# Performance work log

Measured on AMD Instinct MI355X. Metric: run time of the kernel, lower is better.

Reference implementation:

```python
import jax, jax.numpy as jnp
import numpy as np

NUM_HEADS = 16
NUM_KV_HEADS = 4
HEAD_DIM = 128
MAX_LEN = 1024
SEQ_LENS = [1024, 896, 768, 640, 1024, 512, 960, 704]
SCALE = HEAD_DIM ** -0.5
NEG_INF = -1e10  # matches the Triton kernel's masking constant


def setup_inputs() -> dict:
    key = jax.random.key(0)
    kq, kk, kv = jax.random.split(key, 3)
    total = int(np.sum(SEQ_LENS))  # 6528 ragged tokens
    q = jax.random.normal(kq, (total, NUM_HEADS, HEAD_DIM), dtype=jnp.float32)
    k = jax.random.normal(kk, (total, NUM_KV_HEADS, HEAD_DIM), dtype=jnp.float32)
    v = jax.random.normal(kv, (total, NUM_KV_HEADS, HEAD_DIM), dtype=jnp.float32)
    cu_seqlens = jnp.asarray(np.concatenate([[0], np.cumsum(SEQ_LENS)]), dtype=jnp.int32)
    return {"q": q, "k": k, "v": v, "cu_seqlens": cu_seqlens}


def _varlen_flash_attention(q, k, v, cu_seqlens):
    # q: [T, H, D]; k, v: [T, KVH, D]; cu_seqlens: [B+1]
    T, H, D = q.shape
    KVH = k.shape[1]
    g = H // KVH  # GQA group size; head h reads kv head h // g (consecutive groups)
    lens = cu_seqlens[1:] - cu_seqlens[:-1]                 # [B]
    pos = jnp.arange(MAX_LEN)
    idx = cu_seqlens[:-1, None] + pos[None, :]              # [B, L] ragged -> padded gather indices
    valid = pos[None, :] < lens[:, None]                    # [B, L]
    idx = jnp.where(valid, idx, 0)
    qp = q[idx]                                             # [B, L, H, D]
    kp = jnp.repeat(k[idx], g, axis=2)                      # [B, L, H, D]
    vp = jnp.repeat(v[idx], g, axis=2)                      # [B, L, H, D]
    scores = jnp.einsum('blhd,bmhd->bhlm', qp, kp) * SCALE  # [B, H, L, L]
    causal = pos[:, None] >= pos[None, :]                   # [L, L]
    mask = causal[None, None, :, :] & valid[:, None, None, :]
    scores = jnp.where(mask, scores, NEG_INF)
    p = jax.nn.softmax(scores, axis=-1)                     # stable online-softmax equivalent
    op = jnp.einsum('bhlm,bmhd->blhd', p, vp)               # [B, L, H, D]
    op = op * valid[..., None, None]                        # zero padded query rows
    # scatter padded output back to ragged layout (each valid idx is unique)
    out = jnp.zeros_like(q).at[idx.reshape(-1)].add(op.reshape(-1, H, D))
    return out


def reference(q, k, v, cu_seqlens):
    return _varlen_flash_attention(q, k, v, cu_seqlens)
```

## Files before the change

### kernel.cpp

```cpp
#include <hip/hip_runtime.h>
#include <stdint.h>


#define NH 16
#define NKVH 4
#define HD 128
#define NB 8
#define SCALE 0.08838834764831844f
#define NEG_INF -1.0e10f
#define NT32 204
#define TILE_IMG 32768
#define WS_NEED ((size_t)NKVH * NT32 * TILE_IMG)

typedef short bf16x8 __attribute__((ext_vector_type(8)));
typedef float f32x16 __attribute__((ext_vector_type(16)));
typedef unsigned short us4 __attribute__((ext_vector_type(4)));
typedef unsigned short us8 __attribute__((ext_vector_type(8)));

union FragU { us8 u; bf16x8 b; };

__device__ __forceinline__ unsigned short f2bf(float f) {
    uint32_t u = __float_as_uint(f);
    u += 0x7fffu + ((u >> 16) & 1u);
    return (unsigned short)(u >> 16);
}
__device__ __forceinline__ float bf2f(unsigned short h) {
    return __uint_as_float(((uint32_t)h) << 16);
}

__constant__ int c_s32[NB] = {0, 32, 60, 84, 104, 136, 152, 182};
__constant__ signed char c_b[NT32] = {
  0,4, 0,4, 0,4,6, 0,4,6, 0,1,4,6, 0,1,4,6, 0,1,4,6, 0,1,4,6,
  0,1,2,4,6, 0,1,2,4,6, 0,1,2,4,6,7, 0,1,2,4,6,7,
  0,1,2,3,4,6,7, 0,1,2,3,4,6,7, 0,1,2,3,4,6,7, 0,1,2,3,4,6,7,
  0,1,2,3,4,5,6,7, 0,1,2,3,4,5,6,7, 0,1,2,3,4,5,6,7, 0,1,2,3,4,5,6,7,
  0,1,2,3,4,5,6,7, 0,1,2,3,4,5,6,7, 0,1,2,3,4,5,6,7, 0,1,2,3,4,5,6,7,
  0,1,2,3,4,5,6,7, 0,1,2,3,4,5,6,7, 0,1,2,3,4,5,6,7, 0,1,2,3,4,5,6,7,
  0,1,2,3,4,5,6,7, 0,1,2,3,4,5,6,7, 0,1,2,3,4,5,6,7, 0,1,2,3,4,5,6,7};
__constant__ signed char c_qt[NT32] = {
  31,31, 30,30, 29,29,29, 28,28,28, 27,27,27,27, 26,26,26,26, 25,25,25,25,
  24,24,24,24, 23,23,23,23,23, 22,22,22,22,22, 21,21,21,21,21,21,
  20,20,20,20,20,20, 19,19,19,19,19,19,19, 18,18,18,18,18,18,18,
  17,17,17,17,17,17,17, 16,16,16,16,16,16,16,
  15,15,15,15,15,15,15,15, 14,14,14,14,14,14,14,14, 13,13,13,13,13,13,13,13,
  12,12,12,12,12,12,12,12, 11,11,11,11,11,11,11,11, 10,10,10,10,10,10,10,10,
  9,9,9,9,9,9,9,9, 8,8,8,8,8,8,8,8, 7,7,7,7,7,7,7,7, 6,6,6,6,6,6,6,6,
  5,5,5,5,5,5,5,5, 4,4,4,4,4,4,4,4, 3,3,3,3,3,3,3,3, 2,2,2,2,2,2,2,2,
  1,1,1,1,1,1,1,1, 0,0,0,0,0,0,0,0};

__global__ __launch_bounds__(256, 4)
void prepack(const float* __restrict__ K, const float* __restrict__ V,
             unsigned char* __restrict__ ws)
{
    const int gt  = blockIdx.x;
    const int kvh = blockIdx.y;
    const int tid = threadIdx.x;
    unsigned char* img = ws + ((size_t)(kvh * NT32 + gt)) * TILE_IMG;

    #pragma unroll
    for (int i = 0; i < 4; ++i) {
        int chunk = tid + 256 * i;
        int key = chunk >> 5, dq = chunk & 31;
        const float* kp = K + ((size_t)(gt * 32 + key) * NKVH + kvh) * HD + dq * 4;
        float4 f = *reinterpret_cast<const float4*>(kp);
        us4 hi4, lo4;
        hi4[0]=f2bf(f.x); hi4[1]=f2bf(f.y); hi4[2]=f2bf(f.z); hi4[3]=f2bf(f.w);
        lo4[0]=f2bf(f.x-bf2f(hi4[0])); lo4[1]=f2bf(f.y-bf2f(hi4[1]));
        lo4[2]=f2bf(f.z-bf2f(hi4[2])); lo4[3]=f2bf(f.w-bf2f(hi4[3]));
        int off = (key * 256 + dq * 8) ^ ((key & 7) << 4);
        *reinterpret_cast<us4*>(img + off)        = hi4;
        *reinterpret_cast<us4*>(img + 8192 + off) = lo4;
    }
    {
        const int d = tid & 127, g2 = tid >> 7;
        const float* vp = V + ((size_t)(gt * 32 + g2 * 16) * NKVH + kvh) * HD + d;
        #pragma unroll
        for (int m = 0; m < 4; ++m) {
            float f0 = vp[(m*4+0) * (NKVH*HD)];
            float f1 = vp[(m*4+1) * (NKVH*HD)];
            float f2 = vp[(m*4+2) * (NKVH*HD)];
            float f3 = vp[(m*4+3) * (NKVH*HD)];
            us4 hi4, lo4;
            hi4[0]=f2bf(f0); hi4[1]=f2bf(f1); hi4[2]=f2bf(f2); hi4[3]=f2bf(f3);
            lo4[0]=f2bf(f0-bf2f(hi4[0])); lo4[1]=f2bf(f1-bf2f(hi4[1]));
            lo4[2]=f2bf(f2-bf2f(hi4[2])); lo4[3]=f2bf(f3-bf2f(hi4[3]));
            int off = (d * 64 + (g2 * 16 + m * 4) * 2) ^ ((d & 7) << 4);
            *reinterpret_cast<us4*>(img + 16384 + off) = hi4;
            *reinterpret_cast<us4*>(img + 24576 + off) = lo4;
        }
    }
}

#define GLOAD_LDS(g, l) \
    __builtin_amdgcn_global_load_lds((const __attribute__((address_space(1))) void*)(g), \
                                     (__attribute__((address_space(3))) void*)(l), 16, 0, 0)

__global__ __launch_bounds__(256, 2)
void fa_fwd_ws(const float* __restrict__ Q, const unsigned char* __restrict__ ws,
               float* __restrict__ O)
{
    __shared__ unsigned char smem[2][TILE_IMG];

    const int bx  = blockIdx.x;
    const int kvh = blockIdx.y;
    const int b   = c_b[bx], qt = c_qt[bx];
    const int gx  = c_s32[b] + qt;
    const int nt  = qt + 1;

    const int tid  = threadIdx.x;
    const int w    = tid >> 6;
    const int lane = tid & 63;
    const int c    = lane & 31;
    const int hib  = lane >> 5;
    const int swz  = (c & 7) << 4;
    const int hi16 = hib << 4;

    const int head  = kvh * 4 + w;
    const int token = gx * 32 + c;

    const unsigned char* imgbase = ws + (size_t)(kvh * NT32 + c_s32[b]) * TILE_IMG;

    bf16x8 qfh[8], qfl[8];
    {
        const float* qp = Q + ((size_t)token * NH + head) * HD + (hib ? 8 : 0);
        #pragma unroll
        for (int ks = 0; ks < 8; ++ks) {
            float4 f0 = *reinterpret_cast<const float4*>(qp + ks * 16);
            float4 f1 = *reinterpret_cast<const float4*>(qp + ks * 16 + 4);
            float e[8] = {f0.x, f0.y, f0.z, f0.w, f1.x, f1.y, f1.z, f1.w};
            FragU uh, ul;
            #pragma unroll
            for (int j = 0; j < 8; ++j) {
                float s = e[j] * SCALE;
                unsigned short h = f2bf(s);
                uh.u[j] = h;
                ul.u[j] = f2bf(s - bf2f(h));
            }
            qfh[ks] = uh.b; qfl[ks] = ul.b;
        }
    }

    f32x16 oacc[4];
    #pragma unroll
    for (int d = 0; d < 4; ++d)
        #pragma unroll
        for (int r = 0; r < 16; ++r) oacc[d][r] = 0.f;
    float mrun = -1.0e30f, lrun = 0.f;

    #pragma unroll
    for (int j = 0; j < 8; ++j)
        GLOAD_LDS(imgbase + j * 4096 + w * 1024 + (lane << 4),
                  &smem[0][j * 4096 + w * 1024]);

    for (int t = 0; t < nt; ++t) {
        const int buf = t & 1;
        __syncthreads();
        if (t + 1 < nt) {
            const unsigned char* img = imgbase + (size_t)(t + 1) * TILE_IMG;
            #pragma unroll
            for (int j = 0; j < 8; ++j)
                GLOAD_LDS(img + j * 4096 + w * 1024 + (lane << 4),
                          &smem[buf ^ 1][j * 4096 + w * 1024]);
        }
        const unsigned char* bufp = smem[buf];

        f32x16 sacc;
        #pragma unroll
        for (int r = 0; r < 16; ++r) sacc[r] = 0.f;
        __builtin_amdgcn_s_setprio(1);
        #pragma unroll
        for (int ks = 0; ks < 8; ++ks) {
            int koff = (c * 256 + ks * 32 + hi16) ^ swz;
            bf16x8 kh = *reinterpret_cast<const bf16x8*>(bufp + koff);
            bf16x8 kl = *reinterpret_cast<const bf16x8*>(bufp + 8192 + koff);
            sacc = __builtin_amdgcn_mfma_f32_32x32x16_bf16(kh, qfh[ks], sacc, 0, 0, 0);
            sacc = __builtin_amdgcn_mfma_f32_32x32x16_bf16(kl, qfh[ks], sacc, 0, 0, 0);
            sacc = __builtin_amdgcn_mfma_f32_32x32x16_bf16(kh, qfl[ks], sacc, 0, 0, 0);
        }
        __builtin_amdgcn_s_setprio(0);

        if (t == nt - 1) {
            #pragma unroll
            for (int r = 0; r < 16; ++r) {
                int keyl = (r & 3) + 8 * (r >> 2) + 4 * hib;
                if (keyl > c) sacc[r] = NEG_INF;
            }
        }

        float tm = -1.0e30f;
        #pragma unroll
        for (int r = 0; r < 16; ++r) tm = fmaxf(tm, sacc[r]);
        tm = fmaxf(tm, __shfl_xor(tm, 32));
        const float mnew = fmaxf(mrun, tm);
        const float corr = __expf(mrun - mnew);
        float psum = 0.f;
        #pragma unroll
        for (int r = 0; r < 16; ++r) {
            float e = __expf(sacc[r] - mnew);
            sacc[r] = e;
            psum += e;
        }
        psum += __shfl_xor(psum, 32);
        lrun = lrun * corr + psum;
        mrun = mnew;
        #pragma unroll
        for (int d = 0; d < 4; ++d)
            #pragma unroll
            for (int r = 0; r < 16; ++r) oacc[d][r] *= corr;

        bf16x8 pfh[2], pfl[2];
        #pragma unroll
        for (int s = 0; s < 2; ++s) {
            FragU uh, ul;
            #pragma unroll
            for (int bb = 0; bb < 4; ++bb) {
                float own  = hib ? sacc[8*s + 4 + bb] : sacc[8*s + bb];
                float send = hib ? sacc[8*s + bb]     : sacc[8*s + 4 + bb];
                float x = __shfl_xor(send, 32);
                float e0 = hib ? x : own;
                float e1 = hib ? own : x;
                unsigned short h0_ = f2bf(e0), h1_ = f2bf(e1);
                uh.u[bb]     = h0_; ul.u[bb]     = f2bf(e0 - bf2f(h0_));
                uh.u[4 + bb] = h1_; ul.u[4 + bb] = f2bf(e1 - bf2f(h1_));
            }
            pfh[s] = uh.b; pfl[s] = ul.b;
        }

        __builtin_amdgcn_s_setprio(1);
        #pragma unroll
        for (int db = 0; db < 4; ++db) {
            #pragma unroll
            for (int s = 0; s < 2; ++s) {
                int voff = ((db * 32 + c) * 64 + s * 32 + hi16) ^ swz;
                bf16x8 vh = *reinterpret_cast<const bf16x8*>(bufp + 16384 + voff);
                bf16x8 vl = *reinterpret_cast<const bf16x8*>(bufp + 24576 + voff);
                oacc[db] = __builtin_amdgcn_mfma_f32_32x32x16_bf16(vh, pfh[s], oacc[db], 0, 0, 0);
                oacc[db] = __builtin_amdgcn_mfma_f32_32x32x16_bf16(vl, pfh[s], oacc[db], 0, 0, 0);
                oacc[db] = __builtin_amdgcn_mfma_f32_32x32x16_bf16(vh, pfl[s], oacc[db], 0, 0, 0);
            }
        }
        __builtin_amdgcn_s_setprio(0);
    }

    const float inv = 1.f / lrun;
    float* op = O + ((size_t)token * NH + head) * HD;
    #pragma unroll
    for (int db = 0; db < 4; ++db)
        #pragma unroll
        for (int i = 0; i < 4; ++i) {
            float4 r;
            r.x = oacc[db][4*i+0] * inv;
            r.y = oacc[db][4*i+1] * inv;
            r.z = oacc[db][4*i+2] * inv;
            r.w = oacc[db][4*i+3] * inv;
            *reinterpret_cast<float4*>(op + db * 32 + 8 * i + 4 * hib) = r;
        }
}

__constant__ int c_cu_fb[NB + 1] = {0, 1024, 1920, 2688, 3328, 4352, 4864, 5824, 6528};
__constant__ signed char c_pb_fb[102] = {
  0,4, 0,4,6, 0,1,4,6, 0,1,4,6, 0,1,2,4,6, 0,1,2,4,6,7,
  0,1,2,3,4,6,7, 0,1,2,3,4,6,7, 0,1,2,3,4,5,6,7, 0,1,2,3,4,5,6,7,
  0,1,2,3,4,5,6,7, 0,1,2,3,4,5,6,7, 0,1,2,3,4,5,6,7, 0,1,2,3,4,5,6,7,
  0,1,2,3,4,5,6,7, 0,1,2,3,4,5,6,7};
__constant__ signed char c_pqt_fb[102] = {
  15,15, 14,14,14, 13,13,13,13, 12,12,12,12, 11,11,11,11,11, 10,10,10,10,10,10,
  9,9,9,9,9,9,9, 8,8,8,8,8,8,8, 7,7,7,7,7,7,7,7, 6,6,6,6,6,6,6,6,
  5,5,5,5,5,5,5,5, 4,4,4,4,4,4,4,4, 3,3,3,3,3,3,3,3, 2,2,2,2,2,2,2,2,
  1,1,1,1,1,1,1,1, 0,0,0,0,0,0,0,0};

union SharedU {
    struct { unsigned short kh[64 * 128], kl[64 * 128], vh[128 * 64], vl[128 * 64]; } kv;
    struct { float o[4][32 * 132]; } ep;
};

__global__ __launch_bounds__(256, 2)
void fa_fwd_fb(const float* __restrict__ Q, const float* __restrict__ K,
               const float* __restrict__ V, float* __restrict__ O)
{
    __shared__ SharedU smem;
    const int b    = c_pb_fb[blockIdx.x];
    const int qt   = c_pqt_fb[blockIdx.x];
    const int seq0 = c_cu_fb[b];
    const int q0   = qt * 64;
    const int nt   = qt + 1;
    const int hk = blockIdx.y >> 1;
    const int h0 = hk * 4 + (blockIdx.y & 1) * 2;
    const int tid  = threadIdx.x;
    const int w    = tid >> 6;
    const int lane = tid & 63;
    const int c    = lane & 31;
    const int hib  = lane >> 5;
    const int c7   = c & 7;
    const int hi16 = hib << 4;
    const int head  = h0 + (w >> 1);
    const int qbase = q0 + (w & 1) * 32;
    const int qpos  = qbase + c;

    bf16x8 qfh[8], qfl[8];
    {
        const float* qp = Q + ((size_t)(seq0 + qbase + c) * NH + head) * HD + (hib ? 8 : 0);
        #pragma unroll
        for (int ks = 0; ks < 8; ++ks) {
            float4 f0 = *reinterpret_cast<const float4*>(qp + ks * 16);
            float4 f1 = *reinterpret_cast<const float4*>(qp + ks * 16 + 4);
            float e[8] = {f0.x, f0.y, f0.z, f0.w, f1.x, f1.y, f1.z, f1.w};
            FragU uh, ul;
            #pragma unroll
            for (int j = 0; j < 8; ++j) {
                float s = e[j] * SCALE;
                unsigned short h = f2bf(s);
                uh.u[j] = h; ul.u[j] = f2bf(s - bf2f(h));
            }
            qfh[ks] = uh.b; qfl[ks] = ul.b;
        }
    }
    f32x16 oacc[4];
    #pragma unroll
    for (int d = 0; d < 4; ++d)
        #pragma unroll
        for (int r = 0; r < 16; ++r) oacc[d][r] = 0.f;
    float mrun = -1.0e30f, lrun = 0.f;

    for (int t = 0; t < nt; ++t) {
        const int kg0 = seq0 + t * 64;
        __syncthreads();
        #pragma unroll
        for (int i = 0; i < 8; ++i) {
            int chunk = tid + 256 * i;
            int key = chunk >> 5, dq = chunk & 31;
            const float* kp = K + ((size_t)(kg0 + key) * NKVH + hk) * HD + dq * 4;
            float4 f = *reinterpret_cast<const float4*>(kp);
            us4 hi4, lo4;
            hi4[0]=f2bf(f.x); hi4[1]=f2bf(f.y); hi4[2]=f2bf(f.z); hi4[3]=f2bf(f.w);
            lo4[0]=f2bf(f.x-bf2f(hi4[0])); lo4[1]=f2bf(f.y-bf2f(hi4[1]));
            lo4[2]=f2bf(f.z-bf2f(hi4[2])); lo4[3]=f2bf(f.w-bf2f(hi4[3]));
            int off = (key * 256 + dq * 8) ^ ((key & 7) << 4);
            *reinterpret_cast<us4*>((char*)smem.kv.kh + off) = hi4;
            *reinterpret_cast<us4*>((char*)smem.kv.kl + off) = lo4;
        }
        {
            const int d = tid & 127, kb2 = tid >> 7;
            const float* vp = V + ((size_t)(kg0 + kb2 * 32) * NKVH + hk) * HD + d;
            #pragma unroll
            for (int mq = 0; mq < 8; ++mq) {
                float f0 = vp[(mq*4+0) * (NKVH*HD)];
                float f1 = vp[(mq*4+1) * (NKVH*HD)];
                float f2 = vp[(mq*4+2) * (NKVH*HD)];
                float f3 = vp[(mq*4+3) * (NKVH*HD)];
                us4 hi4, lo4;
                hi4[0]=f2bf(f0); hi4[1]=f2bf(f1); hi4[2]=f2bf(f2); hi4[3]=f2bf(f3);
                lo4[0]=f2bf(f0-bf2f(hi4[0])); lo4[1]=f2bf(f1-bf2f(hi4[1]));
                lo4[2]=f2bf(f2-bf2f(hi4[2])); lo4[3]=f2bf(f3-bf2f(hi4[3]));
                int off = (d * 128 + (kb2 * 32 + mq * 4) * 2) ^ ((d & 7) << 4);
                *reinterpret_cast<us4*>((char*)smem.kv.vh + off) = hi4;
                *reinterpret_cast<us4*>((char*)smem.kv.vl + off) = lo4;
            }
        }
        __syncthreads();

        f32x16 sacc[2];
        #pragma unroll
        for (int kb = 0; kb < 2; ++kb)
            #pragma unroll
            for (int r = 0; r < 16; ++r) sacc[kb][r] = 0.f;
        #pragma unroll
        for (int ks = 0; ks < 8; ++ks) {
            #pragma unroll
            for (int kb = 0; kb < 2; ++kb) {
                int off = ((kb * 32 + c) * 256 + ks * 32 + hi16) ^ (c7 << 4);
                bf16x8 kh = *reinterpret_cast<bf16x8*>((char*)smem.kv.kh + off);
                bf16x8 kl = *reinterpret_cast<bf16x8*>((char*)smem.kv.kl + off);
                sacc[kb] = __builtin_amdgcn_mfma_f32_32x32x16_bf16(kh, qfh[ks], sacc[kb], 0, 0, 0);
                sacc[kb] = __builtin_amdgcn_mfma_f32_32x32x16_bf16(kl, qfh[ks], sacc[kb], 0, 0, 0);
                sacc[kb] = __builtin_amdgcn_mfma_f32_32x32x16_bf16(kh, qfl[ks], sacc[kb], 0, 0, 0);
            }
        }
        if (t == nt - 1) {
            #pragma unroll
            for (int kb = 0; kb < 2; ++kb)
                #pragma unroll
                for (int r = 0; r < 16; ++r) {
                    int keyl = kb * 32 + (r & 3) + 8 * (r >> 2) + 4 * hib;
                    if (t * 64 + keyl > qpos) sacc[kb][r] = NEG_INF;
                }
        }
        float tm = -1.0e30f;
        #pragma unroll
        for (int kb = 0; kb < 2; ++kb)
            #pragma unroll
            for (int r = 0; r < 16; ++r) tm = fmaxf(tm, sacc[kb][r]);
        tm = fmaxf(tm, __shfl_xor(tm, 32));
        const float mnew = fmaxf(mrun, tm);
        const float corr = __expf(mrun - mnew);
        float psum = 0.f;
        #pragma unroll
        for (int kb = 0; kb < 2; ++kb)
            #pragma unroll
            for (int r = 0; r < 16; ++r) {
                float e = __expf(sacc[kb][r] - mnew);
                sacc[kb][r] = e; psum += e;
            }
        psum += __shfl_xor(psum, 32);
        lrun = lrun * corr + psum;
        mrun = mnew;
        #pragma unroll
        for (int d = 0; d < 4; ++d)
            #pragma unroll
            for (int r = 0; r < 16; ++r) oacc[d][r] *= corr;

        bf16x8 pfh[4], pfl[4];
        #pragma unroll
        for (int s = 0; s < 4; ++s) {
            const int kb = s >> 1, sh = s & 1;
            FragU uh, ul;
            #pragma unroll
            for (int bb = 0; bb < 4; ++bb) {
                float own  = hib ? sacc[kb][8*sh + 4 + bb] : sacc[kb][8*sh + bb];
                float send = hib ? sacc[kb][8*sh + bb]     : sacc[kb][8*sh + 4 + bb];
                float x = __shfl_xor(send, 32);
                float e0 = hib ? x : own;
                float e1 = hib ? own : x;
                unsigned short h0_ = f2bf(e0), h1_ = f2bf(e1);
                uh.u[bb]     = h0_; ul.u[bb]     = f2bf(e0 - bf2f(h0_));
                uh.u[4 + bb] = h1_; ul.u[4 + bb] = f2bf(e1 - bf2f(h1_));
            }
            pfh[s] = uh.b; pfl[s] = ul.b;
        }
        #pragma unroll
        for (int db = 0; db < 4; ++db) {
            #pragma unroll
            for (int s = 0; s < 4; ++s) {
                int off = ((db * 32 + c) * 128 + s * 32 + hi16) ^ (c7 << 4);
                bf16x8 vh = *reinterpret_cast<bf16x8*>((char*)smem.kv.vh + off);
                bf16x8 vl = *reinterpret_cast<bf16x8*>((char*)smem.kv.vl + off);
                oacc[db] = __builtin_amdgcn_mfma_f32_32x32x16_bf16(vh, pfh[s], oacc[db], 0, 0, 0);
                oacc[db] = __builtin_amdgcn_mfma_f32_32x32x16_bf16(vl, pfh[s], oacc[db], 0, 0, 0);
                oacc[db] = __builtin_amdgcn_mfma_f32_32x32x16_bf16(vh, pfl[s], oacc[db], 0, 0, 0);
            }
        }
    }
    __syncthreads();
    {
        const float inv = 1.f / lrun;
        float* orow = smem.ep.o[w];
        #pragma unroll
        for (int db = 0; db < 4; ++db)
            #pragma unroll
            for (int r = 0; r < 16; ++r) {
                int d = db * 32 + (r & 3) + 8 * (r >> 2) + 4 * hib;
                orow[c * 132 + d] = oacc[db][r] * inv;
            }
        #pragma unroll
        for (int i = 0; i < 16; ++i) {
            int chunk = lane + 64 * i;
            int row = chunk >> 5, c16 = chunk & 31;
            float4 val = *reinterpret_cast<float4*>(orow + row * 132 + c16 * 4);
            int qtok = seq0 + qbase + row;
            *reinterpret_cast<float4*>(O + ((size_t)qtok * NH + head) * HD + c16 * 4) = val;
        }
    }
}

extern "C" void kernel_launch(void* const* d_in, const int* in_sizes, int n_in,
                              void* d_out, int out_size, void* d_ws, size_t ws_size,
                              hipStream_t stream) {
    const float* q = (const float*)d_in[0];
    const float* k = (const float*)d_in[1];
    const float* v = (const float*)d_in[2];
    float* out = (float*)d_out;

    if (ws_size >= WS_NEED) {
        dim3 gp(NT32, NKVH, 1);
        hipLaunchKernelGGL(prepack, gp, dim3(256, 1, 1), 0, stream,
                           k, v, (unsigned char*)d_ws);
        dim3 gm(NT32, NKVH, 1);
        hipLaunchKernelGGL(fa_fwd_ws, gm, dim3(256, 1, 1), 0, stream,
                           q, (const unsigned char*)d_ws, out);
    } else {
        dim3 grid(102, 8, 1);
        hipLaunchKernelGGL(fa_fwd_fb, grid, dim3(256, 1, 1), 0, stream,
                           q, k, v, out);
    }
}
```

Measured before the change: 223.8 us.

## Single-buffer LDS for higher occupancy, lazy softmax rescale, LDS-staged V prepack

The attention kernel drops its double-buffered LDS tile for a single 32KB buffer. It now loads each tile synchronously (load, barrier, compute) and raises launch bounds to three blocks per SU, trading prefetch overlap for occupancy. The online softmax skips the max update and accumulator rescale unless some row's tile max exceeds the running max by more than 8, which removes the 64 multiplies per tile in the common case. The V prepack now reads coalesced float4 rows and transposes through shared memory before writing 16-byte chunks, instead of doing strided scalar global reads.

```diff
diff --git a/kernel.cpp b/kernel.cpp
--- a/kernel.cpp
+++ b/kernel.cpp
@@ -52,6 +52,7 @@
 void prepack(const float* __restrict__ K, const float* __restrict__ V,
              unsigned char* __restrict__ ws)
 {
+    __shared__ unsigned char vs[16384];
     const int gt  = blockIdx.x;
     const int kvh = blockIdx.y;
     const int tid = threadIdx.x;
@@ -72,22 +73,30 @@
         *reinterpret_cast<us4*>(img + 8192 + off) = lo4;
     }
     {
-        const int d = tid & 127, g2 = tid >> 7;
-        const float* vp = V + ((size_t)(gt * 32 + g2 * 16) * NKVH + kvh) * HD + d;
-        #pragma unroll
-        for (int m = 0; m < 4; ++m) {
-            float f0 = vp[(m*4+0) * (NKVH*HD)];
-            float f1 = vp[(m*4+1) * (NKVH*HD)];
-            float f2 = vp[(m*4+2) * (NKVH*HD)];
-            float f3 = vp[(m*4+3) * (NKVH*HD)];
-            us4 hi4, lo4;
-            hi4[0]=f2bf(f0); hi4[1]=f2bf(f1); hi4[2]=f2bf(f2); hi4[3]=f2bf(f3);
-            lo4[0]=f2bf(f0-bf2f(hi4[0])); lo4[1]=f2bf(f1-bf2f(hi4[1]));
-            lo4[2]=f2bf(f2-bf2f(hi4[2])); lo4[3]=f2bf(f3-bf2f(hi4[3]));
-            int off = (d * 64 + (g2 * 16 + m * 4) * 2) ^ ((d & 7) << 4);
-            *reinterpret_cast<us4*>(img + 16384 + off) = hi4;
-            *reinterpret_cast<us4*>(img + 24576 + off) = lo4;
-        }
+        const int token = tid >> 3;
+        const int dg    = (tid & 7) * 16;
+        const float* vp = V + ((size_t)(gt * 32 + token) * NKVH + kvh) * HD + dg;
+        #pragma unroll
+        for (int j = 0; j < 4; ++j) {
+            float4 f = *reinterpret_cast<const float4*>(vp + j * 4);
+            float e[4] = {f.x, f.y, f.z, f.w};
+            #pragma unroll
+            for (int q = 0; q < 4; ++q) {
+                int d = dg + j * 4 + q;
+                unsigned short h = f2bf(e[q]);
+                unsigned short l = f2bf(e[q] - bf2f(h));
+                int off = (d * 64 + token * 2) ^ ((d & 7) << 4);
+                *reinterpret_cast<unsigned short*>(vs + off)        = h;
+                *reinterpret_cast<unsigned short*>(vs + 8192 + off) = l;
+            }
+        }
+    }
+    __syncthreads();
+    #pragma unroll
+    for (int i = 0; i < 4; ++i) {
+        int off = i * 4096 + tid * 16;
+        *reinterpret_cast<us8*>(img + 16384 + off) =
+            *reinterpret_cast<const us8*>(vs + off);
     }
 }
 
@@ -95,11 +104,11 @@
     __builtin_amdgcn_global_load_lds((const __attribute__((address_space(1))) void*)(g), \
                                      (__attribute__((address_space(3))) void*)(l), 16, 0, 0)
 
-__global__ __launch_bounds__(256, 2)
+__global__ __launch_bounds__(256, 3)
 void fa_fwd_ws(const float* __restrict__ Q, const unsigned char* __restrict__ ws,
                float* __restrict__ O)
 {
-    __shared__ unsigned char smem[2][TILE_IMG];
+    __shared__ unsigned char smem[TILE_IMG];
 
     const int bx  = blockIdx.x;
     const int kvh = blockIdx.y;
@@ -147,22 +156,14 @@
         for (int r = 0; r < 16; ++r) oacc[d][r] = 0.f;
     float mrun = -1.0e30f, lrun = 0.f;
 
-    #pragma unroll
-    for (int j = 0; j < 8; ++j)
-        GLOAD_LDS(imgbase + j * 4096 + w * 1024 + (lane << 4),
-                  &smem[0][j * 4096 + w * 1024]);
-
     for (int t = 0; t < nt; ++t) {
-        const int buf = t & 1;
+        const unsigned char* img = imgbase + (size_t)t * TILE_IMG;
         __syncthreads();
-        if (t + 1 < nt) {
-            const unsigned char* img = imgbase + (size_t)(t + 1) * TILE_IMG;
-            #pragma unroll
-            for (int j = 0; j < 8; ++j)
-                GLOAD_LDS(img + j * 4096 + w * 1024 + (lane << 4),
-                          &smem[buf ^ 1][j * 4096 + w * 1024]);
-        }
-        const unsigned char* bufp = smem[buf];
+        #pragma unroll
+        for (int j = 0; j < 8; ++j)
+            GLOAD_LDS(img + j * 4096 + w * 1024 + (lane << 4),
+                      &smem[j * 4096 + w * 1024]);
+        __syncthreads();
 
         f32x16 sacc;
         #pragma unroll
@@ -171,8 +172,8 @@
         #pragma unroll
         for (int ks = 0; ks < 8; ++ks) {
             int koff = (c * 256 + ks * 32 + hi16) ^ swz;
-            bf16x8 kh = *reinterpret_cast<const bf16x8*>(bufp + koff);
-            bf16x8 kl = *reinterpret_cast<const bf16x8*>(bufp + 8192 + koff);
+            bf16x8 kh = *reinterpret_cast<const bf16x8*>(smem + koff);
+            bf16x8 kl = *reinterpret_cast<const bf16x8*>(smem + 8192 + koff);
             sacc = __builtin_amdgcn_mfma_f32_32x32x16_bf16(kh, qfh[ks], sacc, 0, 0, 0);
             sacc = __builtin_amdgcn_mfma_f32_32x32x16_bf16(kl, qfh[ks], sacc, 0, 0, 0);
             sacc = __builtin_amdgcn_mfma_f32_32x32x16_bf16(kh, qfl[ks], sacc, 0, 0, 0);
@@ -191,22 +192,25 @@
         #pragma unroll
         for (int r = 0; r < 16; ++r) tm = fmaxf(tm, sacc[r]);
         tm = fmaxf(tm, __shfl_xor(tm, 32));
-        const float mnew = fmaxf(mrun, tm);
-        const float corr = __expf(mrun - mnew);
+        if (!__all(tm <= mrun + 8.f)) {
+            const float mnew = fmaxf(mrun, tm);
+            const float corr = __expf(mrun - mnew);
+            lrun *= corr;
+            #pragma unroll
+            for (int d = 0; d < 4; ++d)
+                #pragma unroll
+                for (int r = 0; r < 16; ++r) oacc[d][r] *= corr;
+            mrun = mnew;
+        }
         float psum = 0.f;
         #pragma unroll
         for (int r = 0; r < 16; ++r) {
-            float e = __expf(sacc[r] - mnew);
+            float e = __expf(sacc[r] - mrun);
             sacc[r] = e;
             psum += e;
         }
         psum += __shfl_xor(psum, 32);
-        lrun = lrun * corr + psum;
-        mrun = mnew;
-        #pragma unroll
-        for (int d = 0; d < 4; ++d)
-            #pragma unroll
-            for (int r = 0; r < 16; ++r) oacc[d][r] *= corr;
+        lrun += psum;
 
         bf16x8 pfh[2], pfl[2];
         #pragma unroll
@@ -232,8 +236,8 @@
             #pragma unroll
             for (int s = 0; s < 2; ++s) {
                 int voff = ((db * 32 + c) * 64 + s * 32 + hi16) ^ swz;
-                bf16x8 vh = *reinterpret_cast<const bf16x8*>(bufp + 16384 + voff);
-                bf16x8 vl = *reinterpret_cast<const bf16x8*>(bufp + 24576 + voff);
+                bf16x8 vh = *reinterpret_cast<const bf16x8*>(smem + 16384 + voff);
+                bf16x8 vl = *reinterpret_cast<const bf16x8*>(smem + 24576 + voff);
                 oacc[db] = __builtin_amdgcn_mfma_f32_32x32x16_bf16(vh, pfh[s], oacc[db], 0, 0, 0);
                 oacc[db] = __builtin_amdgcn_mfma_f32_32x32x16_bf16(vl, pfh[s], oacc[db], 0, 0, 0);
                 oacc[db] = __builtin_amdgcn_mfma_f32_32x32x16_bf16(vh, pfl[s], oacc[db], 0, 0, 0);
```

New measurement: 261.7 us. 1.17x slower.
